# Kernel tuning notes

Measured on AMD Instinct MI355X. Metric: run time of the kernel, lower is better.

The kernel has to match this reference:

```python
import jax, jax.numpy as jnp
import numpy as np

KERNEL_MUL = 2.0
KERNEL_NUM = 5


def setup_inputs() -> dict:
    key = jax.random.key(0)
    k1, k2 = jax.random.split(key)
    source = jax.random.normal(k1, (4096, 512), dtype=jnp.float32)
    target = jax.random.normal(k2, (4096, 512), dtype=jnp.float32)
    return {"source": source, "target": target}


def reference(source, target):
    b = source.shape[0]
    total = jnp.concatenate([source, target], axis=0)  # [N, D]
    n = total.shape[0]
    # pairwise squared L2 via dot-product trick (same math as expand-subtract)
    sq = jnp.sum(total * total, axis=1)  # [N]
    L2 = sq[:, None] + sq[None, :] - 2.0 * (total @ total.T)  # [N, N]
    # bandwidth uses .data in torch -> constant w.r.t. grads
    bw = jax.lax.stop_gradient(jnp.sum(L2)) / (n * n - n)
    bw = bw / (KERNEL_MUL ** (KERNEL_NUM // 2))
    kernels = jnp.zeros_like(L2)
    for i in range(KERNEL_NUM):  # small fixed loop over bandwidths
        kernels = kernels + jnp.exp(-L2 / (bw * (KERNEL_MUL ** i)))
    XX = jnp.mean(kernels[:b, :b])
    YY = jnp.mean(kernels[b:, b:])
    XY = jnp.mean(kernels[:b, b:])
    YX = jnp.mean(kernels[b:, :b])
    return XX + YY - XY - YX
```

## Files before the change

kernel.cpp:

```cpp
#include <hip/hip_runtime.h>
#include <cstdint>
#include <cstddef>


#define D_DIM 512
#define B_ROWS 4096
#define N_ROWS 8192
#define NTILES 64
#define NBLK_MMD 2080

typedef __attribute__((ext_vector_type(4))) int   i32x4;

#define AS1(p) ((const __attribute__((address_space(1))) void*)(p))
#define AS3(p) ((__attribute__((address_space(3))) void*)(p))

__device__ inline float waveReduce(float v) {
    #pragma unroll
    for (int off = 32; off > 0; off >>= 1) v += __shfl_down(v, off, 64);
    return v;
}

__device__ inline int q8(float x) {
    int v = (int)rintf(x * 16.f);
    v = v > 127 ? 127 : v;
    v = v < -127 ? -127 : v;
    return v & 255;
}

__global__ __launch_bounds__(256) void k_rowstats(const float* __restrict__ src,
                                                  const float* __restrict__ tgt,
                                                  unsigned char* __restrict__ Ti8,
                                                  float* __restrict__ sq) {
    int wave = threadIdx.x >> 6;
    int lane = threadIdx.x & 63;
    int row  = blockIdx.x * 4 + wave;
    const float* base = (row < B_ROWS) ? (src + (size_t)row * D_DIM)
                                       : (tgt + (size_t)(row - B_ROWS) * D_DIM);
    float4 a = ((const float4*)base)[lane * 2];
    float4 b = ((const float4*)base)[lane * 2 + 1];
    uint2 o;
    o.x = (unsigned)(q8(a.x) | (q8(a.y) << 8) | (q8(a.z) << 16) | (q8(a.w) << 24));
    o.y = (unsigned)(q8(b.x) | (q8(b.y) << 8) | (q8(b.z) << 16) | (q8(b.w) << 24));
    ((uint2*)(Ti8 + (size_t)row * D_DIM))[lane] = o;
    float s = a.x*a.x + a.y*a.y + a.z*a.z + a.w*a.w
            + b.x*b.x + b.y*b.y + b.z*b.z + b.w*b.w;
    s = waveReduce(s);
    if (lane == 0) sq[row] = s;
}

__global__ __launch_bounds__(256) void k_colsum(const unsigned int* __restrict__ Tu,
                                                int* __restrict__ partial) {
    int t    = threadIdx.x;
    int ci   = t & 127;
    int half = t >> 7;
    int r0   = blockIdx.x * 128 + half;
    int a0 = 0, a1 = 0, a2 = 0, a3 = 0;
    #pragma unroll 4
    for (int j = 0; j < 64; ++j) {
        unsigned int u = Tu[(size_t)(r0 + 2 * j) * 128 + ci];
        a0 += (int)(signed char)(u);
        a1 += (int)(signed char)(u >> 8);
        a2 += (int)(signed char)(u >> 16);
        a3 += (int)(signed char)(u >> 24);
    }
    int base = ((blockIdx.x * 2 + half) * 512) + ci * 4;
    partial[base + 0] = a0;
    partial[base + 1] = a1;
    partial[base + 2] = a2;
    partial[base + 3] = a3;
}

__global__ __launch_bounds__(512) void k_bw(const int* __restrict__ partial,
                                            const float* __restrict__ sq,
                                            float* __restrict__ c16out) {
    int t = threadIdx.x;
    int csum = 0;
    #pragma unroll 8
    for (int i = 0; i < 128; ++i) csum += partial[i * 512 + t];
    float cs = (float)csum * 0.0625f;
    float p = cs * cs;
    float ssq = 0.f;
    #pragma unroll
    for (int i = 0; i < 16; ++i) ssq += sq[t + i * 512];
    __shared__ float r8[8], q8s[8];
    float wp = waveReduce(p);
    float wq = waveReduce(ssq);
    if ((t & 63) == 0) { r8[t >> 6] = wp; q8s[t >> 6] = wq; }
    __syncthreads();
    if (t == 0) {
        double P = 0.0, Q = 0.0;
        #pragma unroll
        for (int i = 0; i < 8; ++i) { P += r8[i]; Q += q8s[i]; }
        double n = (double)N_ROWS;
        double sumL2 = 2.0 * n * Q - 2.0 * P;
        double bw = sumL2 / (n * n - n) / 4.0;
        c16out[0] = (float)(-1.4426950408889634 / (16.0 * bw));
    }
}

__global__ __launch_bounds__(256, 4) void k_mmd(const unsigned char* __restrict__ Ti8,
                                                const float* __restrict__ sq,
                                                const float* __restrict__ c16in,
                                                float* __restrict__ blockpart) {
    int rem = blockIdx.x;
    int ti = 0, rowlen = NTILES;
    while (rem >= rowlen) { rem -= rowlen; rowlen--; ti++; }
    int tj = ti + rem;

    int tid  = threadIdx.x;
    int wave = tid >> 6;
    int lane = tid & 63;
    int waveM = (wave >> 1) * 64;
    int waveN = (wave & 1) * 64;
    int l15   = lane & 15;
    int quad  = lane >> 4;

    __shared__ unsigned char As[128 * 128];
    __shared__ unsigned char Bs[128 * 128];
    __shared__ float sqA[128];
    __shared__ float sqB[128];
    __shared__ float red[4];

    if (tid < 128)       sqA[tid]       = sq[ti * 128 + tid];
    else                 sqB[tid - 128] = sq[tj * 128 + (tid - 128)];
    float c16 = c16in[0];
    float cgq = -2.f * c16 * (1.f / 256.f);

    i32x4 acc[4][4];
    #pragma unroll
    for (int mi = 0; mi < 4; ++mi)
        #pragma unroll
        for (int ni = 0; ni < 4; ++ni)
            acc[mi][ni] = (i32x4){0, 0, 0, 0};

    const unsigned char* Ag = Ti8 + (size_t)ti * 128 * D_DIM;
    const unsigned char* Bg = Ti8 + (size_t)tj * 128 * D_DIM;

    for (int ks = 0; ks < 4; ++ks) {
        int kb = ks * 128;
        #pragma unroll
        for (int it = 0; it < 4; ++it) {
            int c    = it * 256 + tid;
            int row  = c >> 3;
            int sub  = ((c & 7) ^ (row & 7)) << 4;
            int dsub = (c & 7) << 4;
            __builtin_amdgcn_global_load_lds(
                AS1(Ag + (size_t)row * D_DIM + kb + sub),
                AS3(As + row * 128 + dsub), 16, 0, 0);
            __builtin_amdgcn_global_load_lds(
                AS1(Bg + (size_t)row * D_DIM + kb + sub),
                AS3(Bs + row * 128 + dsub), 16, 0, 0);
        }
        __syncthreads();

        #pragma unroll
        for (int kk = 0; kk < 2; ++kk) {
            int cidx = kk * 4 + quad;
            i32x4 af[4], bfr[4];
            #pragma unroll
            for (int mi = 0; mi < 4; ++mi) {
                int r = waveM + mi * 16 + l15;
                af[mi] = *(const i32x4*)(As + r * 128 + ((cidx ^ (r & 7)) << 4));
            }
            #pragma unroll
            for (int ni = 0; ni < 4; ++ni) {
                int r = waveN + ni * 16 + l15;
                bfr[ni] = *(const i32x4*)(Bs + r * 128 + ((cidx ^ (r & 7)) << 4));
            }
            #pragma unroll
            for (int mi = 0; mi < 4; ++mi)
                #pragma unroll
                for (int ni = 0; ni < 4; ++ni)
                    acc[mi][ni] = __builtin_amdgcn_mfma_i32_16x16x64_i8(
                        af[mi], bfr[ni], acc[mi][ni], 0, 0, 0);
        }
        __syncthreads();
    }

    float trow16[16];
    #pragma unroll
    for (int mi = 0; mi < 4; ++mi)
        #pragma unroll
        for (int r = 0; r < 4; ++r)
            trow16[mi * 4 + r] = sqA[waveM + mi * 16 + quad * 4 + r] * c16;
    float tcol16[4];
    #pragma unroll
    for (int ni = 0; ni < 4; ++ni)
        tcol16[ni] = sqB[waveN + ni * 16 + l15] * c16;

    bool dtile = (ti == tj);
    float psum = 0.f;
    #pragma unroll
    for (int mi = 0; mi < 4; ++mi) {
        #pragma unroll
        for (int ni = 0; ni < 4; ++ni) {
            #pragma unroll
            for (int r = 0; r < 4; ++r) {
                float g   = (float)acc[mi][ni][r];
                float t16 = __builtin_fmaf(g, cgq, trow16[mi * 4 + r]) + tcol16[ni];
                float e1  = __builtin_amdgcn_exp2f(t16);
                float e2  = e1 * e1;
                float e4  = e2 * e2;
                float e8  = e4 * e4;
                float e16 = e8 * e8;
                float ks5 = ((e1 + e2) + (e4 + e8)) + e16;
                int rl = waveM + mi * 16 + quad * 4 + r;
                int cl = waveN + ni * 16 + l15;
                psum += (dtile && rl == cl) ? 5.0f : ks5;
            }
        }
    }

    float w = waveReduce(psum);
    if (lane == 0) red[wave] = w;
    __syncthreads();
    if (tid == 0) {
        float tot   = red[0] + red[1] + red[2] + red[3];
        float sign  = ((ti < 32) == (tj < 32)) ? 1.f : -1.f;
        float scale = (ti == tj) ? sign : 2.f * sign;
        blockpart[blockIdx.x] = tot * scale;
    }
}

__global__ __launch_bounds__(256) void k_final(const float* __restrict__ bp,
                                               float* __restrict__ out) {
    int t = threadIdx.x;
    float s = 0.f;
    for (int i = t; i < NBLK_MMD; i += 256) s += bp[i];
    __shared__ float r4[4];
    float w = waveReduce(s);
    if ((t & 63) == 0) r4[t >> 6] = w;
    __syncthreads();
    if (t == 0)
        out[0] = (r4[0] + r4[1] + r4[2] + r4[3]) * (1.f / (4096.f * 4096.f));
}

extern "C" void kernel_launch(void* const* d_in, const int* in_sizes, int n_in,
                              void* d_out, int out_size, void* d_ws, size_t ws_size,
                              hipStream_t stream) {
    const float* src = (const float*)d_in[0];
    const float* tgt = (const float*)d_in[1];

    uint8_t* ws = (uint8_t*)d_ws;
    unsigned char* Ti8 = (unsigned char*)ws;
    size_t off = 4194304;
    float* sq      = (float*)(ws + off); off += 32768;
    int*   partial = (int*)  (ws + off); off += 128 * 512 * 4;
    float* bp      = (float*)(ws + off); off += 8320;
    float* c16     = (float*)(ws + off);

    k_rowstats<<<2048, 256, 0, stream>>>(src, tgt, Ti8, sq);
    k_colsum  <<<64, 256, 0, stream>>>((const unsigned int*)Ti8, partial);
    k_bw      <<<1, 512, 0, stream>>>(partial, sq, c16);
    k_mmd     <<<NBLK_MMD, 256, 0, stream>>>(Ti8, sq, c16, bp);
    k_final   <<<1, 256, 0, stream>>>(bp, (float*)d_out);
}
```

Before: 117.4 us.

## Load int8 MFMA operands directly from global memory, dropping LDS staging

The GEMM main loop no longer stages A/B tiles into LDS with global_load_lds plus barriers. Each lane now reads its MFMA fragments straight from global memory (via L1/L2), fully unrolled over K, and reads the sq values from global too. The launch-bounds occupancy hint is dropped. This removes LDS traffic and synchronisation, but rows are fetched redundantly across waves and the per-lane reads may coalesce less well, with more register pressure from the unrolled loads.

```diff
diff --git a/kernel.cpp b/kernel.cpp
--- a/kernel.cpp
+++ b/kernel.cpp
@@ -9,10 +9,7 @@
 #define NTILES 64
 #define NBLK_MMD 2080
 
-typedef __attribute__((ext_vector_type(4))) int   i32x4;
-
-#define AS1(p) ((const __attribute__((address_space(1))) void*)(p))
-#define AS3(p) ((__attribute__((address_space(3))) void*)(p))
+typedef __attribute__((ext_vector_type(4))) int i32x4;
 
 __device__ inline float waveReduce(float v) {
     #pragma unroll
@@ -98,10 +95,10 @@
     }
 }
 
-__global__ __launch_bounds__(256, 4) void k_mmd(const unsigned char* __restrict__ Ti8,
-                                                const float* __restrict__ sq,
-                                                const float* __restrict__ c16in,
-                                                float* __restrict__ blockpart) {
+__global__ __launch_bounds__(256) void k_mmd(const unsigned char* __restrict__ Ti8,
+                                             const float* __restrict__ sq,
+                                             const float* __restrict__ c16in,
+                                             float* __restrict__ blockpart) {
     int rem = blockIdx.x;
     int ti = 0, rowlen = NTILES;
     while (rem >= rowlen) { rem -= rowlen; rowlen--; ti++; }
@@ -115,17 +112,18 @@
     int l15   = lane & 15;
     int quad  = lane >> 4;
 
-    __shared__ unsigned char As[128 * 128];
-    __shared__ unsigned char Bs[128 * 128];
-    __shared__ float sqA[128];
-    __shared__ float sqB[128];
-    __shared__ float red[4];
-
-    if (tid < 128)       sqA[tid]       = sq[ti * 128 + tid];
-    else                 sqB[tid - 128] = sq[tj * 128 + (tid - 128)];
     float c16 = c16in[0];
     float cgq = -2.f * c16 * (1.f / 256.f);
 
+    const i32x4* arow[4];
+    const i32x4* brow[4];
+    #pragma unroll
+    for (int mi = 0; mi < 4; ++mi)
+        arow[mi] = (const i32x4*)(Ti8 + ((size_t)ti * 128 + waveM + mi * 16 + l15) * D_DIM);
+    #pragma unroll
+    for (int ni = 0; ni < 4; ++ni)
+        brow[ni] = (const i32x4*)(Ti8 + ((size_t)tj * 128 + waveN + ni * 16 + l15) * D_DIM);
+
     i32x4 acc[4][4];
     #pragma unroll
     for (int mi = 0; mi < 4; ++mi)
@@ -133,50 +131,24 @@
         for (int ni = 0; ni < 4; ++ni)
             acc[mi][ni] = (i32x4){0, 0, 0, 0};
 
-    const unsigned char* Ag = Ti8 + (size_t)ti * 128 * D_DIM;
-    const unsigned char* Bg = Ti8 + (size_t)tj * 128 * D_DIM;
-
-    for (int ks = 0; ks < 4; ++ks) {
-        int kb = ks * 128;
-        #pragma unroll
-        for (int it = 0; it < 4; ++it) {
-            int c    = it * 256 + tid;
-            int row  = c >> 3;
-            int sub  = ((c & 7) ^ (row & 7)) << 4;
-            int dsub = (c & 7) << 4;
-            __builtin_amdgcn_global_load_lds(
-                AS1(Ag + (size_t)row * D_DIM + kb + sub),
-                AS3(As + row * 128 + dsub), 16, 0, 0);
-            __builtin_amdgcn_global_load_lds(
-                AS1(Bg + (size_t)row * D_DIM + kb + sub),
-                AS3(Bs + row * 128 + dsub), 16, 0, 0);
-        }
-        __syncthreads();
-
-        #pragma unroll
-        for (int kk = 0; kk < 2; ++kk) {
-            int cidx = kk * 4 + quad;
-            i32x4 af[4], bfr[4];
+    #pragma unroll
+    for (int kk = 0; kk < 8; ++kk) {
+        int c = kk * 4 + quad;
+        i32x4 af[4], bf[4];
+        #pragma unroll
+        for (int mi = 0; mi < 4; ++mi) af[mi] = arow[mi][c];
+        #pragma unroll
+        for (int ni = 0; ni < 4; ++ni) bf[ni] = brow[ni][c];
+        #pragma unroll
+        for (int mi = 0; mi < 4; ++mi)
             #pragma unroll
-            for (int mi = 0; mi < 4; ++mi) {
-                int r = waveM + mi * 16 + l15;
-                af[mi] = *(const i32x4*)(As + r * 128 + ((cidx ^ (r & 7)) << 4));
-            }
-            #pragma unroll
-            for (int ni = 0; ni < 4; ++ni) {
-                int r = waveN + ni * 16 + l15;
-                bfr[ni] = *(const i32x4*)(Bs + r * 128 + ((cidx ^ (r & 7)) << 4));
-            }
-            #pragma unroll
-            for (int mi = 0; mi < 4; ++mi)
-                #pragma unroll
-                for (int ni = 0; ni < 4; ++ni)
-                    acc[mi][ni] = __builtin_amdgcn_mfma_i32_16x16x64_i8(
-                        af[mi], bfr[ni], acc[mi][ni], 0, 0, 0);
-        }
-        __syncthreads();
-    }
-
+            for (int ni = 0; ni < 4; ++ni)
+                acc[mi][ni] = __builtin_amdgcn_mfma_i32_16x16x64_i8(
+                    af[mi], bf[ni], acc[mi][ni], 0, 0, 0);
+    }
+
+    const float* sqA = sq + ti * 128;
+    const float* sqB = sq + tj * 128;
     float trow16[16];
     #pragma unroll
     for (int mi = 0; mi < 4; ++mi)
@@ -211,6 +183,7 @@
         }
     }
 
+    __shared__ float red[4];
     float w = waveReduce(psum);
     if (lane == 0) red[wave] = w;
     __syncthreads();
```

After: 152.0 us. 1.29x slower.
